# Kernel tuning notes

Hardware: AMD Instinct MI355X
Metric: run time of the kernel (lower is better)

## Reference

```python
import jax, jax.numpy as jnp
import numpy as np

GRID = 8          # 8x8 lattice -> L = 64 sites
L = GRID * GRID
PW = 3            # 3x3 plaquettes -> plaquette_size = 9
N_PLAQ = L
LOCAL_DIM = 2
M = 128
BATCH = 2048


def _make_plaquettes():
    # One 3x3 plaquette per site with periodic boundaries, matching typical
    # GPSKet plaquette construction: plaquettes[i] = site indices of plaquette i.
    plqs = np.zeros((N_PLAQ, PW * PW), dtype=np.int32)
    for i in range(GRID):
        for j in range(GRID):
            p = i * GRID + j
            k = 0
            for di in range(PW):
                for dj in range(PW):
                    plqs[p, k] = ((i + di) % GRID) * GRID + ((j + dj) % GRID)
                    k += 1
    return jnp.asarray(plqs)


def setup_inputs() -> dict:
    key = jax.random.key(0)
    k1, k2 = jax.random.split(key)
    inputs = jax.random.randint(k1, (BATCH, L), 0, LOCAL_DIM, dtype=jnp.int32)
    # epsilon: (local_dim, n_plaquettes, M, plaquette_size)
    epsilon = jax.random.normal(k2, (LOCAL_DIM, N_PLAQ, M, PW * PW), dtype=jnp.float32)
    plaquettes = _make_plaquettes()
    return {"inputs": inputs, "plaquettes": plaquettes, "epsilon": epsilon}


def reference(inputs, plaquettes, epsilon):
    # inputs: (B, L) int occupancies (to_indices is identity cast)
    # plaquettes: (P, S) int site indices
    # epsilon: (D, P, M, S)
    P, S = plaquettes.shape
    occ_p = inputs[:, plaquettes]                       # (B, P, S) occupancy at each plaquette site
    eps_t = jnp.transpose(epsilon, (1, 3, 0, 2))        # (P, S, D, M)
    # gather epsilon[occ, p, :, s] for every (b, p, s) -> (B, P, S, M)
    gathered = eps_t[jnp.arange(P)[:, None], jnp.arange(S)[None, :], occ_p]
    site_prod = jnp.prod(gathered, axis=2)              # (B, P, M) product over plaquette sites
    # n_syms = 1 (no_syms): out_transformation sums over (plaquette, M, sym) axes
    return jnp.sum(site_prod, axis=(1, 2))              # (B,)
```

## Files before the change

### kernel.cpp

```cpp
#include <hip/hip_runtime.h>
#include <stdint.h>

#define PW 3
#define S 9
#define LSZ 64
#define NP 64
#define M 128
#define BATCH 2048
#define NPAT 512

__global__ __launch_bounds__(128) void build_table(
    const float* __restrict__ eps,
    float* __restrict__ G)
{
    const int p = blockIdx.x >> 2;
    const int q = blockIdx.x & 3;
    const int t = threadIdx.x;

    __shared__ float As[32][M + 4];
    __shared__ float Bs[4][M + 4];

    const int m = t;
    const float* ep = eps + (size_t)p * (M * S) + (size_t)m * S;
    const int dstride = NP * M * S;

    float e0[S], e1[S];
#pragma unroll
    for (int s = 0; s < S; ++s) {
        e0[s] = ep[s];
        e1[s] = ep[dstride + s];
    }
    float c01[4], c234[8];
#pragma unroll
    for (int i = 0; i < 4; ++i)
        c01[i] = ((i & 1) ? e1[0] : e0[0]) * ((i & 2) ? e1[1] : e0[1]);
#pragma unroll
    for (int i = 0; i < 8; ++i)
        c234[i] = ((i & 1) ? e1[2] : e0[2]) * ((i & 2) ? e1[3] : e0[3]) *
                  ((i & 4) ? e1[4] : e0[4]);
#pragma unroll
    for (int lo = 0; lo < 32; ++lo)
        As[lo][m] = c01[lo & 3] * c234[lo >> 2];

    const float tail = ((q & 1) ? e1[7] : e0[7]) * ((q & 2) ? e1[8] : e0[8]);
#pragma unroll
    for (int hl = 0; hl < 4; ++hl)
        Bs[hl][m] = ((hl & 1) ? e1[5] : e0[5]) * ((hl & 2) ? e1[6] : e0[6]) * tail;

    __syncthreads();

    const int lo = t & 31;
    const int hl = t >> 5;
    const float4* Arow = (const float4*)&As[lo][0];
    const float4* Brow = (const float4*)&Bs[hl][0];
    float acc = 0.f;
#pragma unroll 8
    for (int i = 0; i < M / 4; ++i) {
        float4 a = Arow[i];
        float4 b = Brow[i];
        acc += a.x * b.x + a.y * b.y + a.z * b.z + a.w * b.w;
    }
    const int hi = q * 4 + hl;
    G[p * NPAT + (hi << 5) + lo] = acc;
}

__global__ __launch_bounds__(256) void eval_kernel(
    const int* __restrict__ inputs,
    const int* __restrict__ plq,
    const float* __restrict__ G,
    float* __restrict__ out)
{
    __shared__ int splq[NP * S];
    for (int i = threadIdx.x; i < NP * S; i += 256)
        splq[i] = plq[i];
    __syncthreads();

    const int wave = threadIdx.x >> 6;
    const int lane = threadIdx.x & 63;
    const int b = blockIdx.x * 4 + wave;

    const int v = inputs[b * LSZ + lane];
    const unsigned long long mask = __ballot(v != 0);

    int pat = 0;
#pragma unroll
    for (int s = 0; s < S; ++s) {
        const int site = splq[lane * S + s];
        pat |= (int)((mask >> site) & 1ull) << s;
    }
    float val = G[lane * NPAT + pat];

#pragma unroll
    for (int off = 32; off > 0; off >>= 1)
        val += __shfl_down(val, off, 64);
    if (lane == 0) out[b] = val;
}

extern "C" void kernel_launch(void* const* d_in, const int* in_sizes, int n_in,
                              void* d_out, int out_size, void* d_ws, size_t ws_size,
                              hipStream_t stream) {
    const int*   inputs = (const int*)d_in[0];
    const int*   plq    = (const int*)d_in[1];
    const float* eps    = (const float*)d_in[2];
    float* out = (float*)d_out;
    float* G   = (float*)d_ws;

    build_table<<<NP * 4, 128, 0, stream>>>(eps, G);
    eval_kernel<<<BATCH / 4, 256, 0, stream>>>(inputs, plq, G, out);
}
```

Measured before the change: 60.79 us.

## Fuse table build and evaluation into one cooperative kernel with grid sync

Merges the two kernels into a single cooperative launch. The first 256 blocks build the pattern table, a grid-wide barrier follows, and then all 512 blocks evaluate batch rows. This removes the second kernel launch and the gap between launches. In exchange it pays for a grid sync and a cooperative-launch requirement that all 512 blocks be co-resident, and half the threads idle during the table build.

```diff
diff --git a/kernel.cpp b/kernel.cpp
--- a/kernel.cpp
+++ b/kernel.cpp
@@ -1,5 +1,8 @@
 #include <hip/hip_runtime.h>
+#include <hip/hip_cooperative_groups.h>
 #include <stdint.h>
+
+namespace cg = cooperative_groups;
 
 #define PW 3
 #define S 9
@@ -9,74 +12,78 @@
 #define BATCH 2048
 #define NPAT 512
 
-__global__ __launch_bounds__(128) void build_table(
+__global__ __launch_bounds__(256) void fused_plaquette(
+    const int*   __restrict__ inputs,
+    const int*   __restrict__ plq,
     const float* __restrict__ eps,
-    float* __restrict__ G)
+    float*       __restrict__ G,
+    float*       __restrict__ out)
 {
-    const int p = blockIdx.x >> 2;
-    const int q = blockIdx.x & 3;
+    __shared__ float As[32][M + 4];
+    __shared__ float Bs[4][M + 4];
+    __shared__ int   splq[NP * S];
+
     const int t = threadIdx.x;
 
-    __shared__ float As[32][M + 4];
-    __shared__ float Bs[4][M + 4];
+    for (int i = t; i < NP * S; i += 256)
+        splq[i] = plq[i];
 
-    const int m = t;
-    const float* ep = eps + (size_t)p * (M * S) + (size_t)m * S;
-    const int dstride = NP * M * S;
+    if (blockIdx.x < NP * 4) {
+        const int p = blockIdx.x >> 2;
+        const int q = blockIdx.x & 3;
 
-    float e0[S], e1[S];
+        if (t < M) {
+            const int m = t;
+            const float* ep = eps + (size_t)p * (M * S) + (size_t)m * S;
+            const int dstride = 2 * NP * M * S / 2;
+
+            float e0[S], e1[S];
 #pragma unroll
-    for (int s = 0; s < S; ++s) {
-        e0[s] = ep[s];
-        e1[s] = ep[dstride + s];
+            for (int s = 0; s < S; ++s) {
+                e0[s] = ep[s];
+                e1[s] = ep[dstride + s];
+            }
+            float c01[4], c234[8];
+#pragma unroll
+            for (int i = 0; i < 4; ++i)
+                c01[i] = ((i & 1) ? e1[0] : e0[0]) * ((i & 2) ? e1[1] : e0[1]);
+#pragma unroll
+            for (int i = 0; i < 8; ++i)
+                c234[i] = ((i & 1) ? e1[2] : e0[2]) * ((i & 2) ? e1[3] : e0[3]) *
+                          ((i & 4) ? e1[4] : e0[4]);
+#pragma unroll
+            for (int lo = 0; lo < 32; ++lo)
+                As[lo][m] = c01[lo & 3] * c234[lo >> 2];
+
+            const float tail = ((q & 1) ? e1[7] : e0[7]) * ((q & 2) ? e1[8] : e0[8]);
+#pragma unroll
+            for (int hl = 0; hl < 4; ++hl)
+                Bs[hl][m] = ((hl & 1) ? e1[5] : e0[5]) * ((hl & 2) ? e1[6] : e0[6]) * tail;
+        }
+        __syncthreads();
+
+        if (t < M) {
+            const int lo = t & 31;
+            const int hl = t >> 5;
+            const float4* Arow = (const float4*)&As[lo][0];
+            const float4* Brow = (const float4*)&Bs[hl][0];
+            float acc = 0.f;
+#pragma unroll 8
+            for (int i = 0; i < M / 4; ++i) {
+                float4 a = Arow[i];
+                float4 b = Brow[i];
+                acc += a.x * b.x + a.y * b.y + a.z * b.z + a.w * b.w;
+            }
+            const int hi = q * 4 + hl;
+            G[p * NPAT + (hi << 5) + lo] = acc;
+        }
+        __threadfence();
     }
-    float c01[4], c234[8];
-#pragma unroll
-    for (int i = 0; i < 4; ++i)
-        c01[i] = ((i & 1) ? e1[0] : e0[0]) * ((i & 2) ? e1[1] : e0[1]);
-#pragma unroll
-    for (int i = 0; i < 8; ++i)
-        c234[i] = ((i & 1) ? e1[2] : e0[2]) * ((i & 2) ? e1[3] : e0[3]) *
-                  ((i & 4) ? e1[4] : e0[4]);
-#pragma unroll
-    for (int lo = 0; lo < 32; ++lo)
-        As[lo][m] = c01[lo & 3] * c234[lo >> 2];
 
-    const float tail = ((q & 1) ? e1[7] : e0[7]) * ((q & 2) ? e1[8] : e0[8]);
-#pragma unroll
-    for (int hl = 0; hl < 4; ++hl)
-        Bs[hl][m] = ((hl & 1) ? e1[5] : e0[5]) * ((hl & 2) ? e1[6] : e0[6]) * tail;
+    cg::this_grid().sync();
 
-    __syncthreads();
-
-    const int lo = t & 31;
-    const int hl = t >> 5;
-    const float4* Arow = (const float4*)&As[lo][0];
-    const float4* Brow = (const float4*)&Bs[hl][0];
-    float acc = 0.f;
-#pragma unroll 8
-    for (int i = 0; i < M / 4; ++i) {
-        float4 a = Arow[i];
-        float4 b = Brow[i];
-        acc += a.x * b.x + a.y * b.y + a.z * b.z + a.w * b.w;
-    }
-    const int hi = q * 4 + hl;
-    G[p * NPAT + (hi << 5) + lo] = acc;
-}
-
-__global__ __launch_bounds__(256) void eval_kernel(
-    const int* __restrict__ inputs,
-    const int* __restrict__ plq,
-    const float* __restrict__ G,
-    float* __restrict__ out)
-{
-    __shared__ int splq[NP * S];
-    for (int i = threadIdx.x; i < NP * S; i += 256)
-        splq[i] = plq[i];
-    __syncthreads();
-
-    const int wave = threadIdx.x >> 6;
-    const int lane = threadIdx.x & 63;
+    const int wave = t >> 6;
+    const int lane = t & 63;
     const int b = blockIdx.x * 4 + wave;
 
     const int v = inputs[b * LSZ + lane];
@@ -105,6 +112,8 @@
     float* out = (float*)d_out;
     float* G   = (float*)d_ws;
 
-    build_table<<<NP * 4, 128, 0, stream>>>(eps, G);
-    eval_kernel<<<BATCH / 4, 256, 0, stream>>>(inputs, plq, G, out);
+    void* args[] = { (void*)&inputs, (void*)&plq, (void*)&eps,
+                     (void*)&G, (void*)&out };
+    hipLaunchCooperativeKernel((void*)fused_plaquette,
+                               dim3(BATCH / 4), dim3(256), args, 0, stream);
 }
```

Result: slower. 152.7 us (+151.1%).

## Build full plaquette table per block, splitting site factors across thread halves

Applied to the files above, without the earlier changes.

The table-build kernel now uses one 256-thread block per plaquette instead of four 128-thread blocks. The first half of the threads builds the 32 low-site partial products and the second half builds all 16 high-site partial products. Each thread then computes two dot products that share the same A row. This removes the fourfold redundant recomputation and reloading of the A partial products and epsilon, at the cost of launching only 64 blocks, which leaves fewer blocks than the GPU has compute units.

```diff
diff --git a/kernel.cpp b/kernel.cpp
--- a/kernel.cpp
+++ b/kernel.cpp
@@ -9,59 +9,77 @@
 #define BATCH 2048
 #define NPAT 512
 
-__global__ __launch_bounds__(128) void build_table(
+__global__ __launch_bounds__(256) void build_table(
     const float* __restrict__ eps,
     float* __restrict__ G)
 {
-    const int p = blockIdx.x >> 2;
-    const int q = blockIdx.x & 3;
+    const int p = blockIdx.x;
     const int t = threadIdx.x;
 
     __shared__ float As[32][M + 4];
-    __shared__ float Bs[4][M + 4];
+    __shared__ float Bs[16][M + 4];
 
-    const int m = t;
-    const float* ep = eps + (size_t)p * (M * S) + (size_t)m * S;
     const int dstride = NP * M * S;
 
-    float e0[S], e1[S];
+    if (t < M) {
+        const int m = t;
+        const float* ep = eps + (size_t)p * (M * S) + (size_t)m * S;
+        float e0[5], e1[5];
 #pragma unroll
-    for (int s = 0; s < S; ++s) {
-        e0[s] = ep[s];
-        e1[s] = ep[dstride + s];
+        for (int s = 0; s < 5; ++s) {
+            e0[s] = ep[s];
+            e1[s] = ep[dstride + s];
+        }
+        float c01[4], c234[8];
+#pragma unroll
+        for (int i = 0; i < 4; ++i)
+            c01[i] = ((i & 1) ? e1[0] : e0[0]) * ((i & 2) ? e1[1] : e0[1]);
+#pragma unroll
+        for (int i = 0; i < 8; ++i)
+            c234[i] = ((i & 1) ? e1[2] : e0[2]) * ((i & 2) ? e1[3] : e0[3]) *
+                      ((i & 4) ? e1[4] : e0[4]);
+#pragma unroll
+        for (int lo = 0; lo < 32; ++lo)
+            As[lo][m] = c01[lo & 3] * c234[lo >> 2];
+    } else {
+        const int m = t - M;
+        const float* ep = eps + (size_t)p * (M * S) + (size_t)m * S + 5;
+        float e0[4], e1[4];
+#pragma unroll
+        for (int s = 0; s < 4; ++s) {
+            e0[s] = ep[s];
+            e1[s] = ep[dstride + s];
+        }
+        float c56[4], c78[4];
+#pragma unroll
+        for (int i = 0; i < 4; ++i) {
+            c56[i] = ((i & 1) ? e1[0] : e0[0]) * ((i & 2) ? e1[1] : e0[1]);
+            c78[i] = ((i & 1) ? e1[2] : e0[2]) * ((i & 2) ? e1[3] : e0[3]);
+        }
+#pragma unroll
+        for (int hi = 0; hi < 16; ++hi)
+            Bs[hi][m] = c56[hi & 3] * c78[hi >> 2];
     }
-    float c01[4], c234[8];
-#pragma unroll
-    for (int i = 0; i < 4; ++i)
-        c01[i] = ((i & 1) ? e1[0] : e0[0]) * ((i & 2) ? e1[1] : e0[1]);
-#pragma unroll
-    for (int i = 0; i < 8; ++i)
-        c234[i] = ((i & 1) ? e1[2] : e0[2]) * ((i & 2) ? e1[3] : e0[3]) *
-                  ((i & 4) ? e1[4] : e0[4]);
-#pragma unroll
-    for (int lo = 0; lo < 32; ++lo)
-        As[lo][m] = c01[lo & 3] * c234[lo >> 2];
-
-    const float tail = ((q & 1) ? e1[7] : e0[7]) * ((q & 2) ? e1[8] : e0[8]);
-#pragma unroll
-    for (int hl = 0; hl < 4; ++hl)
-        Bs[hl][m] = ((hl & 1) ? e1[5] : e0[5]) * ((hl & 2) ? e1[6] : e0[6]) * tail;
 
     __syncthreads();
 
-    const int lo = t & 31;
-    const int hl = t >> 5;
-    const float4* Arow = (const float4*)&As[lo][0];
-    const float4* Brow = (const float4*)&Bs[hl][0];
-    float acc = 0.f;
+    const int lo  = t & 31;
+    const int hi0 = t >> 5;
+    const int hi1 = hi0 + 8;
+    const float4* Arow  = (const float4*)&As[lo][0];
+    const float4* Brow0 = (const float4*)&Bs[hi0][0];
+    const float4* Brow1 = (const float4*)&Bs[hi1][0];
+    float acc0 = 0.f, acc1 = 0.f;
 #pragma unroll 8
     for (int i = 0; i < M / 4; ++i) {
-        float4 a = Arow[i];
-        float4 b = Brow[i];
-        acc += a.x * b.x + a.y * b.y + a.z * b.z + a.w * b.w;
+        float4 a  = Arow[i];
+        float4 b0 = Brow0[i];
+        float4 b1 = Brow1[i];
+        acc0 += a.x * b0.x + a.y * b0.y + a.z * b0.z + a.w * b0.w;
+        acc1 += a.x * b1.x + a.y * b1.y + a.z * b1.z + a.w * b1.w;
     }
-    const int hi = q * 4 + hl;
-    G[p * NPAT + (hi << 5) + lo] = acc;
+    G[p * NPAT + t]       = acc0;
+    G[p * NPAT + t + 256] = acc1;
 }
 
 __global__ __launch_bounds__(256) void eval_kernel(
@@ -105,6 +123,6 @@
     float* out = (float*)d_out;
     float* G   = (float*)d_ws;
 
-    build_table<<<NP * 4, 128, 0, stream>>>(eps, G);
+    build_table<<<NP, 256, 0, stream>>>(eps, G);
     eval_kernel<<<BATCH / 4, 256, 0, stream>>>(inputs, plq, G, out);
 }
```

After: 61.57 us. No clear change (+1.3%).
